# Kernel optimization log

Measured on AMD Instinct MI355X. Metric: run time of the kernel, lower is better.

The kernel has to match this reference:

```python
import jax, jax.numpy as jnp
import numpy as np

HIDDEN = 1024
NUM_HEADS = 16
B, S = 2, 2048


def _mha(x, w_in, b_in, w_out, b_out, num_heads):
    # x: [..., L, E]; standard nn.MultiheadAttention math (eval mode, no dropout)
    lead = x.shape[:-2]
    L, E = x.shape[-2], x.shape[-1]
    dh = E // num_heads
    qkv = x @ w_in.T + b_in                      # [..., L, 3E]
    q, k, v = jnp.split(qkv, 3, axis=-1)
    q = q.reshape(lead + (L, num_heads, dh)) * (dh ** -0.5)
    k = k.reshape(lead + (L, num_heads, dh))
    v = v.reshape(lead + (L, num_heads, dh))
    scores = jnp.einsum('...qhd,...khd->...hqk', q, k)
    probs = jax.nn.softmax(scores, axis=-1)
    out = jnp.einsum('...hqk,...khd->...qhd', probs, v).reshape(lead + (L, E))
    return out @ w_out.T + b_out


def setup_inputs() -> dict:
    key = jax.random.key(0)
    ks = jax.random.split(key, 12)
    E = HIDDEN
    s_in = 1.0 / np.sqrt(E)
    inp = {
        'x': jax.random.normal(ks[0], (B, S, E), dtype=jnp.float32),
        'w_in_g': jax.random.normal(ks[1], (3 * E, E), dtype=jnp.float32) * s_in,
        'b_in_g': jnp.zeros((3 * E,), dtype=jnp.float32),
        'w_out_g': jax.random.normal(ks[2], (E, E), dtype=jnp.float32) * s_in,
        'b_out_g': jnp.zeros((E,), dtype=jnp.float32),
        'w_in_l': jax.random.normal(ks[3], (3 * E, E), dtype=jnp.float32) * s_in,
        'b_in_l': jnp.zeros((3 * E,), dtype=jnp.float32),
        'w_out_l': jax.random.normal(ks[4], (E, E), dtype=jnp.float32) * s_in,
        'b_out_l': jnp.zeros((E,), dtype=jnp.float32),
        'w_f': jax.random.normal(ks[5], (E, 2 * E), dtype=jnp.float32) * (1.0 / np.sqrt(2 * E)),
        'b_f': jnp.zeros((E,), dtype=jnp.float32),
    }
    return inp


def reference(x, w_in_g, b_in_g, w_out_g, b_out_g,
              w_in_l, b_in_l, w_out_l, b_out_l, w_f, b_f):
    Bn, Sn, E = x.shape
    # global full attention over the whole sequence
    g = _mha(x, w_in_g, b_in_g, w_out_g, b_out_g, NUM_HEADS)   # [B,S,E]
    # block-local attention: blocks of length num_heads along the sequence
    sub_len = NUM_HEADS
    sub_num = Sn // sub_len
    xb = x.reshape(Bn, sub_num, sub_len, E)
    l = _mha(xb, w_in_l, b_in_l, w_out_l, b_out_l, NUM_HEADS).reshape(Bn, Sn, E)
    fused = jnp.concatenate([g, l], axis=-1)                   # [B,S,2E]
    return fused @ w_f.T + b_f
```

## Files before the change

kernel.cpp:

```cpp
#include <hip/hip_runtime.h>
#include <hip/hip_bf16.h>
#include <math.h>
#include <stdint.h>

constexpr int Bz = 2;
constexpr int S  = 2048;
constexpr int E  = 1024;
constexpr int NH = 16;
constexpr int DH = 64;
constexpr int QS = 6144;

typedef __attribute__((ext_vector_type(8))) short short8;
typedef __attribute__((ext_vector_type(4))) float f32x4;
typedef __attribute__((ext_vector_type(8))) unsigned short bf16x8;
typedef __attribute__((ext_vector_type(4))) unsigned short bf16x4;

__device__ __forceinline__ float bf2f(unsigned short u) {
    union { unsigned int i; float f; } c; c.i = ((unsigned int)u) << 16; return c.f;
}
__device__ __forceinline__ unsigned short f2bf(float f) {
    union { float f; unsigned int i; } c; c.f = f;
    unsigned int r = c.i + 0x7fffu + ((c.i >> 16) & 1u);
    return (unsigned short)(r >> 16);
}

__device__ __forceinline__ void pack4_store(unsigned short* dst,
                                            float a, float b, float c, float d) {
#if __has_builtin(__builtin_amdgcn_cvt_pk_bf16_f32)
    auto p0 = __builtin_amdgcn_cvt_pk_bf16_f32(a, b);
    auto p1 = __builtin_amdgcn_cvt_pk_bf16_f32(c, d);
    union { decltype(p0) v; unsigned int u; } c0, c1;
    c0.v = p0; c1.v = p1;
    uint2 w; w.x = c0.u; w.y = c1.u;
    *(uint2*)dst = w;
#else
    bf16x4 o = { f2bf(a), f2bf(b), f2bf(c), f2bf(d) };
    *(bf16x4*)dst = o;
#endif
}

#define GLD_LDS(g, l) __builtin_amdgcn_global_load_lds( \
    (const __attribute__((address_space(1))) void*)(g), \
    (__attribute__((address_space(3))) void*)(l), 16, 0, 0)

struct PrepArgs {
    const float* csrc[4]; unsigned short* cdst[4]; int cn[4];
    const float* wog; const float* wol;
    unsigned short* wogT; unsigned short* wolT;
    const float* wf; const float* bf; const float* bog; const float* bol;
    float* cb;
};

__global__ __launch_bounds__(256)
void prep_all(PrepArgs a)
{
    __shared__ unsigned short T[64][72];
    const int bid = blockIdx.x, t = threadIdx.x;

    if (bid < 12288) {
        int i = (bid * 256 + t) * 4;
        #pragma unroll
        for (int r = 0; r < 4; ++r) {
            if (i < a.cn[r]) {
                float4 v = *(const float4*)(a.csrc[r] + i);
                bf16x4 o = { f2bf(v.x), f2bf(v.y), f2bf(v.z), f2bf(v.w) };
                *(bf16x4*)(a.cdst[r] + i) = o;
                return;
            }
            i -= a.cn[r];
        }
        return;
    }
    if (bid < 12800) {
        const int id = bid - 12288;
        const int tj = id & 15, ti = (id >> 4) & 15, mat = id >> 8;
        const float* src = mat ? a.wol : a.wog;
        unsigned short* dst = mat ? a.wolT : a.wogT;
        #pragma unroll
        for (int r = 0; r < 4; ++r) {
            const int c = r * 256 + t;
            const int row = c >> 4, col4 = (c & 15) * 4;
            float4 v = *(const float4*)(src + (size_t)(ti * 64 + row) * 1024 + tj * 64 + col4);
            T[col4 + 0][row] = f2bf(v.x);
            T[col4 + 1][row] = f2bf(v.y);
            T[col4 + 2][row] = f2bf(v.z);
            T[col4 + 3][row] = f2bf(v.w);
        }
        __syncthreads();
        #pragma unroll
        for (int r = 0; r < 2; ++r) {
            const int c = r * 256 + t;
            const int jrow = c >> 3, ig = (c & 7) * 8;
            bf16x8 o;
            #pragma unroll
            for (int k = 0; k < 8; ++k) o[k] = T[jrow][ig + k];
            *(bf16x8*)(dst + (size_t)(tj * 64 + jrow) * 1024 + ti * 64 + ig) = o;
        }
        return;
    }
    {
        const int lane = t & 63;
        const int n = (bid - 12800) * 4 + (t >> 6);
        const float* row = a.wf + (size_t)n * 2048;
        float s = 0.f;
        #pragma unroll
        for (int i = 0; i < 16; ++i) s = fmaf(row[i * 64 + lane], a.bog[i * 64 + lane], s);
        #pragma unroll
        for (int i = 16; i < 32; ++i) s = fmaf(row[i * 64 + lane], a.bol[i * 64 + lane - 1024], s);
        #pragma unroll
        for (int off = 32; off > 0; off >>= 1) s += __shfl_xor(s, off, 64);
        if (lane == 0) a.cb[n] = a.bf[n] + s;
    }
}

struct GemmFusedArgs {
    const unsigned short* xb;    const unsigned short* win;
    const unsigned short* wfb;   const unsigned short* woutT;
    const float* bg;             const float* bl;
    unsigned short* qkv;  unsigned short* vt;  unsigned short* vtl;
    unsigned short* wcomb;
};

__global__ __launch_bounds__(256, 2)
void gemm_fused(GemmFusedArgs g)
{
    __shared__ __align__(16) short As[128 * 64];
    __shared__ __align__(16) short Bs[128 * 64];

    const int bid = blockIdx.x;
    const unsigned short *A, *W;
    unsigned short *C, *vt, *vtl;
    const float *bias0, *bias1;
    int m0, n0, lda, ldw, ldc, nsplit;

    if (bid < 1536) {
        m0 = (bid / 48) * 128;  n0 = (bid % 48) * 128;
        A = g.xb;  W = g.win;  C = g.qkv;  vt = g.vt;  vtl = g.vtl;
        bias0 = g.bg;  bias1 = g.bl;
        lda = 1024;  ldw = 1024;  ldc = QS;  nsplit = 3072;
    } else {
        const int id = bid - 1536;
        const int z = id >> 6;
        m0 = ((id >> 3) & 7) * 128;  n0 = (id & 7) * 128;
        A = g.wfb + z * 1024;
        W = g.woutT + (size_t)z * 1024 * 1024;
        C = g.wcomb + z * 1024;
        vt = nullptr;  vtl = nullptr;  bias0 = nullptr;  bias1 = nullptr;
        lda = 2048;  ldw = 1024;  ldc = 2048;  nsplit = 0;
    }

    const int t = threadIdx.x;
    const int lane = t & 63, wave = t >> 6;
    const int wm = wave & 1, wn = wave >> 1;
    const int lm = lane & 15, lk = lane >> 4;

    f32x4 acc[4][4] = {};

    const int row0 = t >> 3, kg0 = (t & 7) * 8;
    const unsigned short* a0 = A + (size_t)(m0 + row0) * lda + kg0;
    const unsigned short* w0 = W + (size_t)(n0 + row0) * ldw + kg0;

    for (int k0 = 0; k0 < 1024; k0 += 64) {
        __syncthreads();
        #pragma unroll
        for (int r = 0; r < 4; ++r)
            GLD_LDS(a0 + (size_t)(r * 32) * lda + k0, As + ((size_t)(r * 256 + wave * 64)) * 8);
        #pragma unroll
        for (int r = 0; r < 4; ++r)
            GLD_LDS(w0 + (size_t)(r * 32) * ldw + k0, Bs + ((size_t)(r * 256 + wave * 64)) * 8);
        __syncthreads();

        #pragma unroll
        for (int ks = 0; ks < 2; ++ks) {
            short8 af[4], bfr[4];
            #pragma unroll
            for (int i = 0; i < 4; ++i)
                af[i] = *(const short8*)&As[(wm * 64 + i * 16 + lm) * 64 + ks * 32 + lk * 8];
            #pragma unroll
            for (int j = 0; j < 4; ++j)
                bfr[j] = *(const short8*)&Bs[(wn * 64 + j * 16 + lm) * 64 + ks * 32 + lk * 8];
            #pragma unroll
            for (int i = 0; i < 4; ++i)
                #pragma unroll
                for (int j = 0; j < 4; ++j)
                    acc[i][j] = __builtin_amdgcn_mfma_f32_16x16x32_bf16(af[i], bfr[j], acc[i][j], 0, 0, 0);
        }
    }

    #pragma unroll
    for (int i = 0; i < 4; ++i) {
        #pragma unroll
        for (int j = 0; j < 4; ++j) {
            const int nn = n0 + wn * 64 + j * 16 + lm;
            const float bv = (nn < nsplit) ? (bias0 ? bias0[nn] : 0.f)
                                           : (bias1 ? bias1[nn - nsplit] : 0.f);
            const int mm0 = m0 + wm * 64 + i * 16 + lk * 4;
            float vv[4];
            const bool deadC = vt && ((nn >= 2048 && nn < 3072) || nn >= 5120);
            #pragma unroll
            for (int r = 0; r < 4; ++r) {
                vv[r] = acc[i][j][r] + bv;
                if (!deadC) C[(size_t)(mm0 + r) * ldc + nn] = f2bf(vv[r]);
            }
            if (vt) {
                const int nl = nn - 2048;
                if (nl >= 0 && nl < 1024) {
                    const int hh = nl >> 6, dd = nl & 63;
                    const int bb = mm0 >> 11, ss = mm0 & 2047;
                    pack4_store(vt + ((size_t)(bb * NH + hh) * 64 + dd) * S + ss,
                                vv[0], vv[1], vv[2], vv[3]);
                }
                const int nl2 = nn - 5120;
                if (nl2 >= 0) {
                    const int hh = nl2 >> 6, dd = nl2 & 63;
                    const int bb = mm0 >> 11, ss = mm0 & 2047;
                    pack4_store(vtl + ((size_t)(bb * NH + hh) * 64 + dd) * S + ss,
                                vv[0], vv[1], vv[2], vv[3]);
                }
            }
        }
    }
}

__global__ __launch_bounds__(256, 2)
void gemm_tail(const unsigned short* __restrict__ A, const unsigned short* __restrict__ W,
               const float* __restrict__ bias, float* __restrict__ C)
{
    __shared__ __align__(16) short As[128 * 64];
    __shared__ __align__(16) short Bs[64 * 64];

    const int t = threadIdx.x;
    const int lane = t & 63, wave = t >> 6;
    const int wm = wave & 1, wn = wave >> 1;
    const int m0 = blockIdx.y * 128, n0 = blockIdx.x * 64;
    const int lm = lane & 15, lk = lane >> 4;

    f32x4 acc[4][2] = {};

    const int row0 = t >> 3, kg0 = (t & 7) * 8;
    const unsigned short* a0 = A + (size_t)(m0 + row0) * 2048 + kg0;
    const unsigned short* w0 = W + (size_t)(n0 + row0) * 2048 + kg0;

    for (int k0 = 0; k0 < 2048; k0 += 64) {
        __syncthreads();
        #pragma unroll
        for (int r = 0; r < 4; ++r)
            GLD_LDS(a0 + (size_t)(r * 32) * 2048 + k0, As + ((size_t)(r * 256 + wave * 64)) * 8);
        #pragma unroll
        for (int r = 0; r < 2; ++r)
            GLD_LDS(w0 + (size_t)(r * 32) * 2048 + k0, Bs + ((size_t)(r * 256 + wave * 64)) * 8);
        __syncthreads();

        #pragma unroll
        for (int ks = 0; ks < 2; ++ks) {
            short8 af[4], bfr[2];
            #pragma unroll
            for (int i = 0; i < 4; ++i)
                af[i] = *(const short8*)&As[(wm * 64 + i * 16 + lm) * 64 + ks * 32 + lk * 8];
            #pragma unroll
            for (int j = 0; j < 2; ++j)
                bfr[j] = *(const short8*)&Bs[(wn * 32 + j * 16 + lm) * 64 + ks * 32 + lk * 8];
            #pragma unroll
            for (int i = 0; i < 4; ++i)
                #pragma unroll
                for (int j = 0; j < 2; ++j)
                    acc[i][j] = __builtin_amdgcn_mfma_f32_16x16x32_bf16(af[i], bfr[j], acc[i][j], 0, 0, 0);
        }
    }

    #pragma unroll
    for (int i = 0; i < 4; ++i) {
        #pragma unroll
        for (int j = 0; j < 2; ++j) {
            const int nn = n0 + wn * 32 + j * 16 + lm;
            const float bv = bias[nn];
            const int mm0 = m0 + wm * 64 + i * 16 + lk * 4;
            #pragma unroll
            for (int r = 0; r < 4; ++r)
                C[(size_t)(mm0 + r) * 1024 + nn] = acc[i][j][r] + bv;
        }
    }
}

__global__ __launch_bounds__(256, 2)
void attn_fused(const unsigned short* __restrict__ qkv,
                const unsigned short* __restrict__ vt,
                const unsigned short* __restrict__ vtl,
                unsigned short* __restrict__ attn)
{
    __shared__ __align__(16) unsigned short Ks[2][64][32];
    __shared__ __align__(16) unsigned short Vs[2][64][32];
    __shared__ __align__(16) unsigned short Pt[4][2][16][64];

    const int t = threadIdx.x, lane = t & 63, wq = t >> 6;
    const int lm = lane & 15, lk = lane >> 4;

    if (blockIdx.x < 512) {
        const int bid = blockIdx.x;
        const int slot = bid >> 3;
        const int p  = (bid & 7) * 4 + (slot >> 4);
        const int qb = slot & 15;
        const int h  = p & 15;
        const int b  = p >> 4;
        const int q0 = qb * 128 + wq * 32;

        constexpr float QSCALE = 0.125f * 1.44269504088896340736f;
        short8 qf[2][2];
        #pragma unroll
        for (int qg = 0; qg < 2; ++qg) {
            const unsigned short* qrow = qkv + ((size_t)(b * S) + q0 + qg * 16 + lm) * QS + h * DH;
            #pragma unroll
            for (int kk = 0; kk < 2; ++kk) {
                bf16x8 v = *(const bf16x8*)(qrow + kk * 32 + lk * 8);
                #pragma unroll
                for (int j = 0; j < 8; ++j)
                    ((unsigned short*)&qf[qg][kk])[j] = f2bf(bf2f(v[j]) * QSCALE);
            }
        }

        short8 ones;
        #pragma unroll
        for (int j = 0; j < 8; ++j) ((unsigned short*)&ones)[j] = 0x3F80;

        const int row0 = t >> 2;
        const int sw0 = (row0 ^ (row0 >> 2)) & 3;
        const int g0 = ((t & 3) ^ sw0) * 8;
        const unsigned short* kg[2];
        const unsigned short* vg[2];
        #pragma unroll
        for (int r = 0; r < 2; ++r) {
            kg[r] = qkv + ((size_t)(b * S) + row0) * QS + E + h * 64 + r * 32 + g0;
            vg[r] = vt + ((size_t)(b * NH + h) * 64 + row0) * S + r * 32 + g0;
        }
        unsigned short* kl[2] = { &Ks[0][0][0] + (wq * 64) * 8, &Ks[0][0][0] + (256 + wq * 64) * 8 };
        unsigned short* vl[2] = { &Vs[0][0][0] + (wq * 64) * 8, &Vs[0][0][0] + (256 + wq * 64) * 8 };

        f32x4 O[2][4] = {};
        f32x4 lacc[2] = {};
        const int sw = lm & 7;
        const int fr = (lm ^ (lm >> 2)) & 3;

        for (int kt = 0; kt < 32; ++kt) {
            __syncthreads();
            GLD_LDS(kg[0] + (size_t)kt * 64 * QS, kl[0]);
            GLD_LDS(kg[1] + (size_t)kt * 64 * QS, kl[1]);
            GLD_LDS(vg[0] + kt * 64, vl[0]);
            GLD_LDS(vg[1] + kt * 64, vl[1]);
            __syncthreads();

            f32x4 st[2][4];
            #pragma unroll
            for (int qg = 0; qg < 2; ++qg)
                #pragma unroll
                for (int jn = 0; jn < 4; ++jn)
                    st[qg][jn] = (f32x4){ -16.f, -16.f, -16.f, -16.f };
            #pragma unroll
            for (int jn = 0; jn < 4; ++jn) {
                #pragma unroll
                for (int kk = 0; kk < 2; ++kk) {
                    short8 kf = *(const short8*)&Ks[kk][jn * 16 + lm][(lk ^ fr) * 8];
                    #pragma unroll
                    for (int qg = 0; qg < 2; ++qg)
                        st[qg][jn] = __builtin_amdgcn_mfma_f32_16x16x32_bf16(kf, qf[qg][kk], st[qg][jn], 0, 0, 0);
                }
            }

            #pragma unroll
            for (int qg = 0; qg < 2; ++qg)
                #pragma unroll
                for (int jn = 0; jn < 4; ++jn) {
                    const int cc = ((jn * 2 + (lk >> 1)) ^ sw) * 8 + (lk & 1) * 4;
                    pack4_store(&Pt[wq][qg][lm][cc],
                                exp2f(st[qg][jn][0]), exp2f(st[qg][jn][1]),
                                exp2f(st[qg][jn][2]), exp2f(st[qg][jn][3]));
                }

            short8 pf[2][2];
            #pragma unroll
            for (int qg = 0; qg < 2; ++qg) {
                pf[qg][0] = *(const short8*)&Pt[wq][qg][lm][((lk + 0) ^ sw) * 8];
                pf[qg][1] = *(const short8*)&Pt[wq][qg][lm][((lk + 4) ^ sw) * 8];
            }

            #pragma unroll
            for (int qg = 0; qg < 2; ++qg)
                #pragma unroll
                for (int kk = 0; kk < 2; ++kk)
                    lacc[qg] = __builtin_amdgcn_mfma_f32_16x16x32_bf16(ones, pf[qg][kk], lacc[qg], 0, 0, 0);

            #pragma unroll
            for (int jd = 0; jd < 4; ++jd) {
                #pragma unroll
                for (int kk = 0; kk < 2; ++kk) {
                    short8 vf = *(const short8*)&Vs[kk][jd * 16 + lm][(lk ^ fr) * 8];
                    #pragma unroll
                    for (int qg = 0; qg < 2; ++qg)
                        O[qg][jd] = __builtin_amdgcn_mfma_f32_16x16x32_bf16(vf, pf[qg][kk], O[qg][jd], 0, 0, 0);
                }
            }
        }

        #pragma unroll
        for (int qg = 0; qg < 2; ++qg) {
            const int q = q0 + qg * 16 + lm;
            const float inv = 1.0f / lacc[qg][0];
            unsigned short* dst = attn + ((size_t)(b * S) + q) * 2048 + h * 64 + lk * 4;
            #pragma unroll
            for (int jd = 0; jd < 4; ++jd)
                pack4_store(dst + jd * 16,
                            O[qg][jd][0] * inv, O[qg][jd][1] * inv,
                            O[qg][jd][2] * inv, O[qg][jd][3] * inv);
        }
        return;
    }

    unsigned short (*PtL)[16][32] = (unsigned short(*)[16][32])&Pt[0][0][0][0];
    const unsigned short* qkvl = qkv + 3072;
    const int gid = (blockIdx.x - 512) * 4 + wq;
    const int h   = gid & 15;
    const int sub = (gid >> 4) & 127;
    const int b   = gid >> 11;
    const int s0  = sub * 16;

    const unsigned short* base = qkvl + ((size_t)(b * S) + s0 + lm) * QS;
    f32x4 st = {};
    #pragma unroll
    for (int kk = 0; kk < 2; ++kk) {
        short8 kf = *(const short8*)(base + E + h * 64 + kk * 32 + lk * 8);
        short8 qf = *(const short8*)(base +     h * 64 + kk * 32 + lk * 8);
        st = __builtin_amdgcn_mfma_f32_16x16x32_bf16(kf, qf, st, 0, 0, 0);
    }

    constexpr float SC = 0.125f * 1.44269504088896340736f;
    float tt[4];
    #pragma unroll
    for (int r = 0; r < 4; ++r) tt[r] = st[r] * SC;
    float mx = fmaxf(fmaxf(tt[0], tt[1]), fmaxf(tt[2], tt[3]));
    mx = fmaxf(mx, __shfl_xor(mx, 16, 64));
    mx = fmaxf(mx, __shfl_xor(mx, 32, 64));
    float p[4], l = 0.f;
    #pragma unroll
    for (int r = 0; r < 4; ++r) { p[r] = exp2f(tt[r] - mx); l += p[r]; }
    l += __shfl_xor(l, 16, 64);
    l += __shfl_xor(l, 32, 64);
    const float inv = 1.0f / l;

    pack4_store(&PtL[wq][lm][lk * 4], p[0], p[1], p[2], p[3]);
    pack4_store(&PtL[wq][lm][16 + lk * 4], 0.f, 0.f, 0.f, 0.f);
    short8 pf = *(const short8*)&PtL[wq][lm][lk * 8];

    const unsigned short* vrow =
        vtl + (((size_t)(b * NH + h) * 64) + lm) * S + s0 + (lk & 1) * 8;
    f32x4 zero = {};
    unsigned short* dst = attn + ((size_t)(b * S) + s0 + lm) * 2048 + 1024 + h * 64 + lk * 4;
    #pragma unroll
    for (int jd = 0; jd < 4; ++jd) {
        short8 vf = *(const short8*)(vrow + (size_t)jd * 16 * S);
        f32x4 O = __builtin_amdgcn_mfma_f32_16x16x32_bf16(vf, pf, zero, 0, 0, 0);
        pack4_store(dst + jd * 16, O[0] * inv, O[1] * inv, O[2] * inv, O[3] * inv);
    }
}

extern "C" void kernel_launch(void* const* d_in, const int* in_sizes, int n_in,
                              void* d_out, int out_size, void* d_ws, size_t ws_size,
                              hipStream_t stream)
{
    const float* x       = (const float*)d_in[0];
    const float* w_in_g  = (const float*)d_in[1];
    const float* b_in_g  = (const float*)d_in[2];
    const float* w_out_g = (const float*)d_in[3];
    const float* b_out_g = (const float*)d_in[4];
    const float* w_in_l  = (const float*)d_in[5];
    const float* b_in_l  = (const float*)d_in[6];
    const float* w_out_l = (const float*)d_in[7];
    const float* b_out_l = (const float*)d_in[8];
    const float* w_f     = (const float*)d_in[9];
    const float* b_f     = (const float*)d_in[10];
    float* out = (float*)d_out;

    const int M = Bz * S;
    char* p = (char*)d_ws;
    unsigned short* xb       = (unsigned short*)p; p += (size_t)M * 1024 * 2;
    unsigned short* qkv_all  = (unsigned short*)p; p += (size_t)M * QS * 2;
    unsigned short* attn_cat = (unsigned short*)p; p += (size_t)M * 2048 * 2;
    unsigned short* win_all  = (unsigned short*)p; p += (size_t)6144 * 1024 * 2;
    unsigned short* wf_b     = (unsigned short*)p; p += (size_t)1024 * 2048 * 2;
    unsigned short* woutT    = (unsigned short*)p; p += (size_t)2 * 1024 * 1024 * 2;
    unsigned short* wcomb    = (unsigned short*)p; p += (size_t)1024 * 2048 * 2;
    unsigned short* vtbuf    = (unsigned short*)p; p += (size_t)Bz * NH * 64 * S * 2;
    unsigned short* vtlbuf   = (unsigned short*)p; p += (size_t)Bz * NH * 64 * S * 2;
    float*          cb       = (float*)p;          p += 1024 * 4;

    dim3 blk(256);

    PrepArgs pa;
    pa.csrc[0] = x;      pa.cdst[0] = xb;                    pa.cn[0] = M * 1024;
    pa.csrc[1] = w_in_g; pa.cdst[1] = win_all;               pa.cn[1] = 3072 * 1024;
    pa.csrc[2] = w_in_l; pa.cdst[2] = win_all + 3072 * 1024; pa.cn[2] = 3072 * 1024;
    pa.csrc[3] = w_f;    pa.cdst[3] = wf_b;                  pa.cn[3] = 1024 * 2048;
    pa.wog = w_out_g; pa.wol = w_out_l;
    pa.wogT = woutT;  pa.wolT = woutT + 1024 * 1024;
    pa.wf = w_f; pa.bf = b_f; pa.bog = b_out_g; pa.bol = b_out_l; pa.cb = cb;
    prep_all<<<dim3(13056), blk, 0, stream>>>(pa);

    GemmFusedArgs ga;
    ga.xb = xb;  ga.win = win_all;  ga.wfb = wf_b;  ga.woutT = woutT;
    ga.bg = b_in_g;  ga.bl = b_in_l;
    ga.qkv = qkv_all;  ga.vt = vtbuf;  ga.vtl = vtlbuf;  ga.wcomb = wcomb;
    gemm_fused<<<dim3(1664), blk, 0, stream>>>(ga);

    attn_fused<<<dim3(1536), blk, 0, stream>>>(qkv_all, vtbuf, vtlbuf, attn_cat);

    gemm_tail<<<dim3(1024 / 64, M / 128), blk, 0, stream>>>(
        attn_cat, wcomb, cb, out);
}
```

Baseline: 292.2 us.

## Double-buffer K/V tiles in global attention loop and raise occupancy hint

The global-attention branch now keeps two LDS buffers for K and V tiles. It issues the async global-to-LDS load for the next tile before computing on the current one, which drops one of the two barriers per iteration. The intent is to hide global load latency behind the MFMA work. It also raises the launch-bounds min-blocks hint from 2 to 3. That limits registers per thread and may cause spills, while the doubled LDS footprint could limit occupancy.

```diff
diff --git a/kernel.cpp b/kernel.cpp
--- a/kernel.cpp
+++ b/kernel.cpp
@@ -282,14 +282,14 @@
     }
 }
 
-__global__ __launch_bounds__(256, 2)
+__global__ __launch_bounds__(256, 3)
 void attn_fused(const unsigned short* __restrict__ qkv,
                 const unsigned short* __restrict__ vt,
                 const unsigned short* __restrict__ vtl,
                 unsigned short* __restrict__ attn)
 {
-    __shared__ __align__(16) unsigned short Ks[2][64][32];
-    __shared__ __align__(16) unsigned short Vs[2][64][32];
+    __shared__ __align__(16) unsigned short Ks[2][2][64][32];
+    __shared__ __align__(16) unsigned short Vs[2][2][64][32];
     __shared__ __align__(16) unsigned short Pt[4][2][16][64];
 
     const int t = threadIdx.x, lane = t & 63, wq = t >> 6;
@@ -332,21 +332,29 @@
             kg[r] = qkv + ((size_t)(b * S) + row0) * QS + E + h * 64 + r * 32 + g0;
             vg[r] = vt + ((size_t)(b * NH + h) * 64 + row0) * S + r * 32 + g0;
         }
-        unsigned short* kl[2] = { &Ks[0][0][0] + (wq * 64) * 8, &Ks[0][0][0] + (256 + wq * 64) * 8 };
-        unsigned short* vl[2] = { &Vs[0][0][0] + (wq * 64) * 8, &Vs[0][0][0] + (256 + wq * 64) * 8 };
 
         f32x4 O[2][4] = {};
         f32x4 lacc[2] = {};
         const int sw = lm & 7;
         const int fr = (lm ^ (lm >> 2)) & 3;
 
+        {
+            GLD_LDS(kg[0], &Ks[0][0][0][0] + wq * 512);
+            GLD_LDS(kg[1], &Ks[0][1][0][0] + wq * 512);
+            GLD_LDS(vg[0], &Vs[0][0][0][0] + wq * 512);
+            GLD_LDS(vg[1], &Vs[0][1][0][0] + wq * 512);
+        }
+        __syncthreads();
+
         for (int kt = 0; kt < 32; ++kt) {
-            __syncthreads();
-            GLD_LDS(kg[0] + (size_t)kt * 64 * QS, kl[0]);
-            GLD_LDS(kg[1] + (size_t)kt * 64 * QS, kl[1]);
-            GLD_LDS(vg[0] + kt * 64, vl[0]);
-            GLD_LDS(vg[1] + kt * 64, vl[1]);
-            __syncthreads();
+            const int db = kt & 1;
+            if (kt + 1 < 32) {
+                const int sb = db ^ 1;
+                GLD_LDS(kg[0] + (size_t)(kt + 1) * 64 * QS, &Ks[sb][0][0][0] + wq * 512);
+                GLD_LDS(kg[1] + (size_t)(kt + 1) * 64 * QS, &Ks[sb][1][0][0] + wq * 512);
+                GLD_LDS(vg[0] + (kt + 1) * 64,              &Vs[sb][0][0][0] + wq * 512);
+                GLD_LDS(vg[1] + (kt + 1) * 64,              &Vs[sb][1][0][0] + wq * 512);
+            }
 
             f32x4 st[2][4];
             #pragma unroll
@@ -358,7 +366,7 @@
             for (int jn = 0; jn < 4; ++jn) {
                 #pragma unroll
                 for (int kk = 0; kk < 2; ++kk) {
-                    short8 kf = *(const short8*)&Ks[kk][jn * 16 + lm][(lk ^ fr) * 8];
+                    short8 kf = *(const short8*)&Ks[db][kk][jn * 16 + lm][(lk ^ fr) * 8];
                     #pragma unroll
                     for (int qg = 0; qg < 2; ++qg)
                         st[qg][jn] = __builtin_amdgcn_mfma_f32_16x16x32_bf16(kf, qf[qg][kk], st[qg][jn], 0, 0, 0);
@@ -392,12 +400,14 @@
             for (int jd = 0; jd < 4; ++jd) {
                 #pragma unroll
                 for (int kk = 0; kk < 2; ++kk) {
-                    short8 vf = *(const short8*)&Vs[kk][jd * 16 + lm][(lk ^ fr) * 8];
+                    short8 vf = *(const short8*)&Vs[db][kk][jd * 16 + lm][(lk ^ fr) * 8];
                     #pragma unroll
                     for (int qg = 0; qg < 2; ++qg)
                         O[qg][jd] = __builtin_amdgcn_mfma_f32_16x16x32_bf16(vf, pf[qg][kk], O[qg][jd], 0, 0, 0);
                 }
             }
+
+            if (kt + 1 < 32) __syncthreads();
         }
 
         #pragma unroll
```

Result: no change. 296.6 us (+1.5%).

## Split global attention over key range and merge partial outputs

Applied to the files above, without the earlier changes.

The global attention blocks now each cover only half of the key tiles, which doubles the global-attention block count to 1024. Each block writes an unnormalized partial output in bf16 plus its row-sum to workspace. A new merge kernel adds the two partials, divides by the combined sum and writes into the concatenated attention buffer. This is meant to raise parallelism and shorten the per-block serial loop, at the cost of an extra kernel launch, about 16MB of extra partial-output traffic, bf16 rounding of the partials, and a block ordering that no longer groups blocks for cache locality.

```diff
diff --git a/kernel.cpp b/kernel.cpp
--- a/kernel.cpp
+++ b/kernel.cpp
@@ -9,6 +9,8 @@
 constexpr int NH = 16;
 constexpr int DH = 64;
 constexpr int QS = 6144;
+constexpr int NSPLIT = 2;
+constexpr int KT_SPLIT = (S / 64) / NSPLIT;
 
 typedef __attribute__((ext_vector_type(8))) short short8;
 typedef __attribute__((ext_vector_type(4))) float f32x4;
@@ -286,6 +288,7 @@
 void attn_fused(const unsigned short* __restrict__ qkv,
                 const unsigned short* __restrict__ vt,
                 const unsigned short* __restrict__ vtl,
+                unsigned short* __restrict__ opart, float* __restrict__ lbuf,
                 unsigned short* __restrict__ attn)
 {
     __shared__ __align__(16) unsigned short Ks[2][64][32];
@@ -295,13 +298,12 @@
     const int t = threadIdx.x, lane = t & 63, wq = t >> 6;
     const int lm = lane & 15, lk = lane >> 4;
 
-    if (blockIdx.x < 512) {
+    if (blockIdx.x < 1024) {
         const int bid = blockIdx.x;
-        const int slot = bid >> 3;
-        const int p  = (bid & 7) * 4 + (slot >> 4);
-        const int qb = slot & 15;
-        const int h  = p & 15;
-        const int b  = p >> 4;
+        const int split = bid & 1;
+        const int qb = (bid >> 1) & 15;
+        const int h  = (bid >> 5) & 15;
+        const int b  = bid >> 9;
         const int q0 = qb * 128 + wq * 32;
 
         constexpr float QSCALE = 0.125f * 1.44269504088896340736f;
@@ -340,7 +342,7 @@
         const int sw = lm & 7;
         const int fr = (lm ^ (lm >> 2)) & 3;
 
-        for (int kt = 0; kt < 32; ++kt) {
+        for (int kt = split * KT_SPLIT; kt < (split + 1) * KT_SPLIT; ++kt) {
             __syncthreads();
             GLD_LDS(kg[0] + (size_t)kt * 64 * QS, kl[0]);
             GLD_LDS(kg[1] + (size_t)kt * 64 * QS, kl[1]);
@@ -403,20 +405,20 @@
         #pragma unroll
         for (int qg = 0; qg < 2; ++qg) {
             const int q = q0 + qg * 16 + lm;
-            const float inv = 1.0f / lacc[qg][0];
-            unsigned short* dst = attn + ((size_t)(b * S) + q) * 2048 + h * 64 + lk * 4;
+            unsigned short* orow = opart + ((((size_t)split * Bz + b) * NH + h) * S + q) * 64;
             #pragma unroll
             for (int jd = 0; jd < 4; ++jd)
-                pack4_store(dst + jd * 16,
-                            O[qg][jd][0] * inv, O[qg][jd][1] * inv,
-                            O[qg][jd][2] * inv, O[qg][jd][3] * inv);
+                pack4_store(orow + jd * 16 + lk * 4,
+                            O[qg][jd][0], O[qg][jd][1], O[qg][jd][2], O[qg][jd][3]);
+            if (lk == 0)
+                lbuf[(((size_t)split * Bz + b) * NH + h) * S + q] = lacc[qg][0];
         }
         return;
     }
 
     unsigned short (*PtL)[16][32] = (unsigned short(*)[16][32])&Pt[0][0][0][0];
     const unsigned short* qkvl = qkv + 3072;
-    const int gid = (blockIdx.x - 512) * 4 + wq;
+    const int gid = (blockIdx.x - 1024) * 4 + wq;
     const int h   = gid & 15;
     const int sub = (gid >> 4) & 127;
     const int b   = gid >> 11;
@@ -459,6 +461,32 @@
         f32x4 O = __builtin_amdgcn_mfma_f32_16x16x32_bf16(vf, pf, zero, 0, 0, 0);
         pack4_store(dst + jd * 16, O[0] * inv, O[1] * inv, O[2] * inv, O[3] * inv);
     }
+}
+
+__global__ __launch_bounds__(256)
+void attn_merge(const unsigned short* __restrict__ opart, const float* __restrict__ lbuf,
+                unsigned short* __restrict__ attn)
+{
+    const int id = blockIdx.x * 256 + threadIdx.x;
+    const int d8 = id & 7;
+    const int q  = (id >> 3) & (S - 1);
+    const int h  = (id >> 14) & 15;
+    const int b  = id >> 18;
+
+    const size_t base0 = (((size_t)0 * Bz + b) * NH + h) * S + q;
+    const size_t base1 = (((size_t)1 * Bz + b) * NH + h) * S + q;
+    const float inv = 1.0f / (lbuf[base0] + lbuf[base1]);
+
+    bf16x8 o0 = *(const bf16x8*)(opart + base0 * 64 + d8 * 8);
+    bf16x8 o1 = *(const bf16x8*)(opart + base1 * 64 + d8 * 8);
+    unsigned short* dst = attn + ((size_t)(b * S) + q) * 2048 + h * 64 + d8 * 8;
+    #pragma unroll
+    for (int j = 0; j < 8; j += 4)
+        pack4_store(dst + j,
+                    (bf2f(o0[j+0]) + bf2f(o1[j+0])) * inv,
+                    (bf2f(o0[j+1]) + bf2f(o1[j+1])) * inv,
+                    (bf2f(o0[j+2]) + bf2f(o1[j+2])) * inv,
+                    (bf2f(o0[j+3]) + bf2f(o1[j+3])) * inv);
 }
 
 extern "C" void kernel_launch(void* const* d_in, const int* in_sizes, int n_in,
@@ -489,6 +517,8 @@
     unsigned short* wcomb    = (unsigned short*)p; p += (size_t)1024 * 2048 * 2;
     unsigned short* vtbuf    = (unsigned short*)p; p += (size_t)Bz * NH * 64 * S * 2;
     unsigned short* vtlbuf   = (unsigned short*)p; p += (size_t)Bz * NH * 64 * S * 2;
+    unsigned short* opart    = (unsigned short*)p; p += (size_t)NSPLIT * Bz * NH * S * 64 * 2;
+    float*          lbuf     = (float*)p;          p += (size_t)NSPLIT * Bz * NH * S * 4;
     float*          cb       = (float*)p;          p += 1024 * 4;
 
     dim3 blk(256);
@@ -509,7 +539,10 @@
     ga.qkv = qkv_all;  ga.vt = vtbuf;  ga.vtl = vtlbuf;  ga.wcomb = wcomb;
     gemm_fused<<<dim3(1664), blk, 0, stream>>>(ga);
 
-    attn_fused<<<dim3(1536), blk, 0, stream>>>(qkv_all, vtbuf, vtlbuf, attn_cat);
+    attn_fused<<<dim3(2048), blk, 0, stream>>>(
+        qkv_all, vtbuf, vtlbuf, opart, lbuf, attn_cat);
+
+    attn_merge<<<dim3(Bz * NH * S * 8 / 256), blk, 0, stream>>>(opart, lbuf, attn_cat);
 
     gemm_tail<<<dim3(1024 / 64, M / 128), blk, 0, stream>>>(
         attn_cat, wcomb, cb, out);
```

After: 293.2 us. No clear change (+0.3%).
